# Performance work log

Hardware: AMD Instinct MI355X
Metric: run time of the kernel (lower is better)

The kernel has to match this reference:

```python
import jax, jax.numpy as jnp
import numpy as np

B, S, D, H, E = 4, 2048, 512, 8, 4  # batch, seq, embed, heads, expand
HD = D // H


def setup_inputs() -> dict:
    key = jax.random.key(0)
    ks = jax.random.split(key, 9)
    s = lambda k, shape, fan: jax.random.normal(k, shape, jnp.float32) * (fan ** -0.5)
    return {
        "x": jax.random.normal(ks[0], (B, S, D), jnp.float32),
        "Wq": s(ks[1], (D, D), D),
        "Wk": s(ks[2], (D, D), D),
        "Wv": s(ks[3], (D, D), D),
        "Wo": s(ks[4], (D, D), D),
        "W1": s(ks[5], (D, D * E), D),
        "b1": jnp.zeros((D * E,), jnp.float32),
        "W2": s(ks[6], (D * E, D), D * E),
        "b2": jnp.zeros((D,), jnp.float32),
    }


def _encoder_layer(x, Wq, Wk, Wv, Wo, W1, b1, W2, b2):
    # NOTE: source computes InstanceNorm1d twice but discards both results -> no-ops.
    scale = D ** -0.25  # applied to BOTH q and k (net 1/sqrt(embed_dim))
    q = (x @ Wq).reshape(B, S, H, HD).transpose(0, 2, 1, 3) * scale  # [B,H,S,hd]
    k = (x @ Wk).reshape(B, S, H, HD).transpose(0, 2, 1, 3) * scale
    v = (x @ Wv).reshape(B, S, H, HD).transpose(0, 2, 1, 3)
    scores = jnp.einsum('bhqd,bhkd->bhqk', q, k)  # [B,H,S,S]
    attn = jax.nn.softmax(scores, axis=-1)
    o = jnp.einsum('bhqk,bhkd->bhqd', attn, v)  # [B,H,S,hd]
    o = o.transpose(0, 2, 1, 3).reshape(B, S, D)
    x = o @ Wo + x  # residual 1
    h = jax.nn.gelu(x @ W1 + b1, approximate=True)  # torch GELU(approximate='tanh')
    return h @ W2 + b2 + x  # residual 2 (dropout=0, eval)


def reference(x, Wq, Wk, Wv, Wo, W1, b1, W2, b2):
    return _encoder_layer(x, Wq, Wk, Wv, Wo, W1, b1, W2, b2)
```

## Files before the change

kernel.cpp:

```cpp
#include <hip/hip_runtime.h>
#include <hip/hip_bf16.h>


typedef __bf16 bf16;
typedef __attribute__((ext_vector_type(8))) __bf16 bf16x8;
typedef __attribute__((ext_vector_type(4))) __bf16 bf16x4;
typedef __attribute__((ext_vector_type(4))) float f32x4;
typedef __attribute__((ext_vector_type(16))) float f32x16;
typedef __attribute__((ext_vector_type(4))) short s16x4;
typedef __attribute__((ext_vector_type(2))) unsigned int u32x2;
typedef __attribute__((ext_vector_type(4))) unsigned int u32x4;

#define LOG2E 1.4426950408889634f
#define SCORE_SCALE 0.044194173824159216f
#define SCALE_L2E (SCORE_SCALE * LOG2E)
#define FIXED_M 12.0f

#if __has_builtin(__builtin_amdgcn_exp2f)
#define EXP2(x) __builtin_amdgcn_exp2f(x)
#else
#define EXP2(x) exp2f(x)
#endif

__device__ __forceinline__ void gl_lds16(const bf16* g, bf16* l) {
  __builtin_amdgcn_global_load_lds(
      (const __attribute__((address_space(1))) unsigned int*)g,
      (__attribute__((address_space(3))) unsigned int*)l, 16, 0, 0);
}

__device__ __forceinline__ float gelu_tanh(float x) {
  float u = 0.7978845608028654f * (x + 0.044715f * x * x * x);
  float e = EXP2(u * (2.0f * LOG2E));
  float th = 1.0f - 2.0f / (e + 1.0f);
  return 0.5f * x * (1.0f + th);
}

__device__ __forceinline__ f32x4 mfma_bf16(bf16x8 a, bf16x8 b, f32x4 c) {
  return __builtin_amdgcn_mfma_f32_16x16x32_bf16(a, b, c, 0, 0, 0);
}
__device__ __forceinline__ f32x16 mfma32x16(bf16x8 a, bf16x8 b, f32x16 c) {
  return __builtin_amdgcn_mfma_f32_32x32x16_bf16(a, b, c, 0, 0, 0);
}

__device__ __forceinline__ void plswap(unsigned int& a, unsigned int& b) {
  asm volatile("v_permlane32_swap_b32 %0, %1" : "+v"(a), "+v"(b));
}

template <int MODE, typename OutT, int TN>
__global__ __launch_bounds__(256, 2) void gemm_bt(
    const bf16* __restrict__ A, const bf16* __restrict__ Bt,
    OutT* __restrict__ C, const float* __restrict__ bias,
    const float* __restrict__ resf, const bf16* __restrict__ resb,
    int M, int N, int K) {
  constexpr int MI = (TN == 128) ? 4 : 2;
  __shared__ __align__(16) bf16 sA[2][128 * 32];
  __shared__ __align__(16) bf16 sB[2][TN * 32];
  const int tid = threadIdx.x;
  const int lane = tid & 63;
  const int quad = lane >> 4, lc = lane & 15;
  const int wave = tid >> 6;
  const int wr = (TN == 128) ? (wave >> 1) : wave;
  const int wc = (TN == 128) ? (wave & 1) : 0;
  const int m0 = blockIdx.y * 128, n0 = blockIdx.x * TN;

  const int srow = tid >> 2;
  const int kc = (tid & 3) * 8;
  const bf16* Ag1 = A + (size_t)(m0 + srow) * K + kc;
  const bf16* Ag2 = A + (size_t)(m0 + 64 + srow) * K + kc;
  const bf16* Bg1 = Bt + (size_t)(n0 + srow) * K + kc;
  const bf16* Bg2 = Bt + (size_t)(n0 + 64 + srow) * K + kc;
  const int o1 = tid * 8, o2 = (tid + 256) * 8;

  f32x4 acc[MI][4];
#pragma unroll
  for (int mi = 0; mi < MI; ++mi)
#pragma unroll
    for (int ni = 0; ni < 4; ++ni) acc[mi][ni] = (f32x4){0.f, 0.f, 0.f, 0.f};

  gl_lds16(Ag1, sA[0] + o1);
  gl_lds16(Ag2, sA[0] + o2);
  gl_lds16(Bg1, sB[0] + o1);
  if (TN == 128) gl_lds16(Bg2, sB[0] + o2);
  Ag1 += 32; Ag2 += 32; Bg1 += 32; Bg2 += 32;

  const int kIters = K >> 5;
  for (int kt = 0; kt < kIters; ++kt) {
    __syncthreads();
    const bf16* cA = sA[kt & 1];
    const bf16* cB = sB[kt & 1];
    if (kt + 1 < kIters) {
      bf16* nA = sA[(kt + 1) & 1];
      bf16* nB = sB[(kt + 1) & 1];
      gl_lds16(Ag1, nA + o1);
      gl_lds16(Ag2, nA + o2);
      gl_lds16(Bg1, nB + o1);
      if (TN == 128) gl_lds16(Bg2, nB + o2);
      Ag1 += 32; Ag2 += 32; Bg1 += 32; Bg2 += 32;
    }

    bf16x8 af[MI], bfm[4];
#pragma unroll
    for (int i = 0; i < MI; ++i)
      af[i] =
          *(const bf16x8*)(cA + ((wr * (16 * MI) + i * 16 + lc) * 32 + quad * 8));
#pragma unroll
    for (int i = 0; i < 4; ++i)
      bfm[i] = *(const bf16x8*)(cB + ((wc * 64 + i * 16 + lc) * 32 + quad * 8));
#pragma unroll
    for (int mi = 0; mi < MI; ++mi)
#pragma unroll
      for (int ni = 0; ni < 4; ++ni)
        acc[mi][ni] = mfma_bf16(af[mi], bfm[ni], acc[mi][ni]);
  }

#pragma unroll
  for (int mi = 0; mi < MI; ++mi) {
#pragma unroll
    for (int r = 0; r < 4; ++r) {
      const int row = m0 + wr * (16 * MI) + mi * 16 + quad * 4 + r;
#pragma unroll
      for (int ni = 0; ni < 4; ++ni) {
        const int col = n0 + wc * 64 + ni * 16 + lc;
        const size_t idx = (size_t)row * N + col;
        float v = acc[mi][ni][r];
        if (MODE == 1) v += resf[idx];
        if (MODE == 2) v = gelu_tanh(v + bias[col]);
        if (MODE == 3) v += bias[col] + (float)resb[idx];
        C[idx] = (OutT)v;
      }
    }
  }
}

__global__ __launch_bounds__(256, 2) void flash_attn(
    const bf16* __restrict__ QKV, const bf16* __restrict__ Vt,
    bf16* __restrict__ O) {
  const int tid = threadIdx.x;
  const int lane = tid & 63, wave = tid >> 6;
  const int lo5 = lane & 31, hi = lane >> 5;
  const int lin = blockIdx.y * 16 + blockIdx.x;
  const int xcd = lin & 7, slot = lin >> 3;
  const int bh = xcd * 4 + (slot >> 4);
  const int qt = slot & 15;
  const int b = bh >> 3, h = bh & 7;
  const int q0 = qt * 128 + wave * 32;

  __shared__ __align__(16) bf16 sK[3][4096];
  __shared__ __align__(16) bf16 sV[4][4096];

  const bf16* Qrow = QKV + (size_t)(b * 2048 + q0 + lo5) * 1536 + h * 64;
  bf16x8 qf[4];
#pragma unroll
  for (int i = 0; i < 4; ++i) qf[i] = *(const bf16x8*)(Qrow + i * 16 + hi * 8);

  const int colsw = (((lane & 7) ^ (lane >> 3)) << 3);
  const bf16* Kg0 = QKV + (size_t)b * 2048 * 1536 + 512 + (size_t)h * 64 +
                    (size_t)(wave * 16 + (lane >> 3)) * 1536 + colsw;
  const bf16* Vg0 = Vt + (size_t)bh * 64 * 2048 +
                    (size_t)(wave * 16 + (lane >> 3)) * 2048 + colsw;
  const int stag = wave * 1024;
  const int m7 = lo5 & 7;

  f32x16 oacc[2];
  oacc[0] = (f32x16)(0.f);
  oacc[1] = (f32x16)(0.f);
  float rsum = 0.f;

  auto stage = [&](int t) {
    bf16* dk = sK[t % 3] + stag;
    bf16* dv = sV[t & 3] + stag;
    gl_lds16(Kg0 + (size_t)t * 64 * 1536, dk);
    gl_lds16(Kg0 + (size_t)(t * 64 + 8) * 1536, dk + 512);
    gl_lds16(Vg0 + t * 64, dv);
    gl_lds16(Vg0 + t * 64 + 8 * 2048, dv + 512);
  };

  bf16x8 paw[4];

  auto qk_softmax = [&](const bf16* cK) {
#pragma unroll
    for (int hl = 0; hl < 2; ++hl) {
      const int R = hl * 32 + lo5;
      bf16x8 kf0 = *(const bf16x8*)(cK + R * 64 + (((0 + hi) ^ m7) << 3));
      bf16x8 kf1 = *(const bf16x8*)(cK + R * 64 + (((2 + hi) ^ m7) << 3));
      bf16x8 kf2 = *(const bf16x8*)(cK + R * 64 + (((4 + hi) ^ m7) << 3));
      bf16x8 kf3 = *(const bf16x8*)(cK + R * 64 + (((6 + hi) ^ m7) << 3));
      f32x16 st0 = (f32x16)(0.f), st1 = (f32x16)(0.f);
      __builtin_amdgcn_s_setprio(1);
      st0 = mfma32x16(kf0, qf[0], st0);
      st1 = mfma32x16(kf1, qf[1], st1);
      st0 = mfma32x16(kf2, qf[2], st0);
      st1 = mfma32x16(kf3, qf[3], st1);
      __builtin_amdgcn_s_setprio(0);
      f32x16 st = st0 + st1;
      unsigned int q32[4][2];
#pragma unroll
      for (int g = 0; g < 4; ++g) {
        bf16x4 pb;
#pragma unroll
        for (int j = 0; j < 4; ++j) {
          float p = EXP2(st[4 * g + j] * SCALE_L2E - FIXED_M);
          rsum += p;
          pb[j] = (bf16)p;
        }
        u32x2 w2 = __builtin_bit_cast(u32x2, pb);
        q32[g][0] = w2[0];
        q32[g][1] = w2[1];
      }
#pragma unroll
      for (int t = 0; t < 2; ++t) {
        unsigned int a0 = q32[2 * t][0], a1 = q32[2 * t][1];
        unsigned int b0 = q32[2 * t + 1][0], b1 = q32[2 * t + 1][1];
        plswap(a0, b0);
        plswap(a1, b1);
        u32x4 f = {a0, a1, b0, b1};
        paw[hl * 2 + t] = __builtin_bit_cast(bf16x8, f);
      }
    }
  };

  auto pv = [&](const bf16* cV) {
    __builtin_amdgcn_s_setprio(1);
#pragma unroll
    for (int dh = 0; dh < 2; ++dh) {
      const int Rd = dh * 32 + lo5;
#pragma unroll
      for (int w = 0; w < 4; ++w) {
        bf16x8 vf =
            *(const bf16x8*)(cV + Rd * 64 + (((2 * w + hi) ^ m7) << 3));
        oacc[dh] = mfma32x16(paw[w], vf, oacc[dh]);
      }
    }
    __builtin_amdgcn_s_setprio(0);
  };

  stage(0);
  stage(1);
  asm volatile("s_waitcnt vmcnt(4)\ns_barrier" ::: "memory");
  stage(2);
  qk_softmax(sK[0]);

  for (int kt = 1; kt < 32; ++kt) {
    if (kt == 31)
      asm volatile("s_waitcnt vmcnt(0)\ns_barrier" ::: "memory");
    else
      asm volatile("s_waitcnt vmcnt(4)\ns_barrier" ::: "memory");
    if (kt + 2 < 32) stage(kt + 2);
    const bf16* cK = sK[kt % 3];
    const bf16* cVp = sV[(kt + 3) & 3];
    pv(cVp);
    qk_softmax(cK);
  }
  pv(sV[31 & 3]);

  rsum += __shfl_xor(rsum, 32, 64);
  const size_t obase = (size_t)(b * 2048 + q0) * 512 + h * 64;
#pragma unroll
  for (int r = 0; r < 16; ++r) {
    const int qloc = (r & 3) + 8 * (r >> 2) + 4 * hi;
    const float inv = 1.0f / __shfl(rsum, qloc, 64);
#pragma unroll
    for (int dh = 0; dh < 2; ++dh)
      O[obase + (size_t)qloc * 512 + dh * 32 + lo5] =
          (bf16)(oacc[dh][r] * inv);
  }
}

__global__ __launch_bounds__(256) void prep(
    const float* __restrict__ x, const float* __restrict__ Wq,
    const float* __restrict__ Wk, const float* __restrict__ Wv,
    const float* __restrict__ Wo, const float* __restrict__ W1,
    const float* __restrict__ W2, bf16* __restrict__ xb,
    bf16* __restrict__ WqkvT, bf16* __restrict__ WoT, bf16* __restrict__ W1T,
    bf16* __restrict__ W2T) {
  const int bid = blockIdx.x;
  if (bid < 4096) {
    const size_t i = ((size_t)bid * 256 + threadIdx.x) * 4;
    const float4 v = *(const float4*)(x + i);
    bf16x4 o;
    o[0] = (bf16)v.x; o[1] = (bf16)v.y; o[2] = (bf16)v.z; o[3] = (bf16)v.w;
    *(bf16x4*)(xb + i) = o;
    return;
  }
  const int t = bid - 4096;
  const float* in;
  bf16* out;
  int in_ld, out_ld, bx, by;
  if (t < 1024) {
    const int q = t >> 8, r = t & 255;
    bx = r & 15; by = r >> 4; in_ld = 512; out_ld = 512;
    in = (q == 0) ? Wq : (q == 1) ? Wk : (q == 2) ? Wv : Wo;
    out = (q == 0) ? WqkvT
          : (q == 1) ? WqkvT + 512 * 512
          : (q == 2) ? WqkvT + 2 * 512 * 512
                     : WoT;
  } else if (t < 2048) {
    const int r = t - 1024;
    bx = r & 63; by = r >> 6; in_ld = 2048; out_ld = 512;
    in = W1; out = W1T;
  } else {
    const int r = t - 2048;
    bx = r & 15; by = r >> 4; in_ld = 512; out_ld = 2048;
    in = W2; out = W2T;
  }
  __shared__ __align__(16) bf16 tl[32][33];
  const int tx = threadIdx.x & 31, ty = threadIdx.x >> 5;
  const int n0 = bx * 32, k0 = by * 32;
#pragma unroll
  for (int i = 0; i < 4; ++i)
    tl[ty + 8 * i][tx] = (bf16)in[(size_t)(k0 + ty + 8 * i) * in_ld + n0 + tx];
  __syncthreads();
#pragma unroll
  for (int i = 0; i < 4; ++i)
    out[(size_t)(n0 + ty + 8 * i) * out_ld + k0 + tx] = tl[tx][ty + 8 * i];
}

__global__ __launch_bounds__(256) void transpose_v(
    const bf16* __restrict__ QKV, bf16* __restrict__ Vt) {
  __shared__ __align__(16) bf16 t[32][33];
  const int tx = threadIdx.x & 31, ty = threadIdx.x >> 5;
  const int bh = blockIdx.z, b = bh >> 3, h = bh & 7;
  const bf16* ip = QKV + (size_t)b * 2048 * 1536 + 1024 + h * 64;
  bf16* op = Vt + (size_t)bh * 64 * 2048;
  const int d0 = blockIdx.x * 32, s0 = blockIdx.y * 32;
#pragma unroll
  for (int i = 0; i < 4; ++i)
    t[ty + 8 * i][tx] = ip[(size_t)(s0 + ty + 8 * i) * 1536 + d0 + tx];
  __syncthreads();
#pragma unroll
  for (int i = 0; i < 4; ++i)
    op[(size_t)(d0 + ty + 8 * i) * 2048 + s0 + tx] = t[tx][ty + 8 * i];
}

extern "C" void kernel_launch(void* const* d_in, const int* in_sizes, int n_in,
                              void* d_out, int out_size, void* d_ws,
                              size_t ws_size, hipStream_t stream) {
  const float* x = (const float*)d_in[0];
  const float* Wq = (const float*)d_in[1];
  const float* Wk = (const float*)d_in[2];
  const float* Wv = (const float*)d_in[3];
  const float* Wo = (const float*)d_in[4];
  const float* W1 = (const float*)d_in[5];
  const float* b1 = (const float*)d_in[6];
  const float* W2 = (const float*)d_in[7];
  const float* b2 = (const float*)d_in[8];
  float* out = (float*)d_out;

  char* ws = (char*)d_ws;
  size_t off = 0;
  auto alloc = [&](size_t bytes) {
    char* p = ws + off;
    off += (bytes + 255) & ~(size_t)255;
    return p;
  };
  bf16* WqkvT = (bf16*)alloc(1536ULL * 512 * 2);
  bf16* WoT = (bf16*)alloc(512ULL * 512 * 2);
  bf16* W1T = (bf16*)alloc(2048ULL * 512 * 2);
  bf16* W2T = (bf16*)alloc(512ULL * 2048 * 2);
  bf16* xb = (bf16*)alloc(8192ULL * 512 * 2);
  bf16* QKV = (bf16*)alloc(8192ULL * 1536 * 2);
  bf16* Vt = (bf16*)alloc(32ULL * 64 * 2048 * 2);
  bf16* attn = (bf16*)alloc(8192ULL * 512 * 2);
  bf16* x2 = xb;
  bf16* hbuf = QKV;

  const dim3 tb(256);
  prep<<<dim3(7168), tb, 0, stream>>>(x, Wq, Wk, Wv, Wo, W1, W2, xb, WqkvT,
                                      WoT, W1T, W2T);
  gemm_bt<0, bf16, 128><<<dim3(12, 64), tb, 0, stream>>>(
      xb, WqkvT, QKV, nullptr, nullptr, nullptr, 8192, 1536, 512);
  transpose_v<<<dim3(2, 64, 32), tb, 0, stream>>>(QKV, Vt);
  flash_attn<<<dim3(16, 32), tb, 0, stream>>>(QKV, Vt, attn);
  gemm_bt<1, bf16, 64><<<dim3(8, 64), tb, 0, stream>>>(
      attn, WoT, x2, nullptr, x, nullptr, 8192, 512, 512);
  gemm_bt<2, bf16, 128><<<dim3(16, 64), tb, 0, stream>>>(
      x2, W1T, hbuf, b1, nullptr, nullptr, 8192, 2048, 512);
  gemm_bt<3, float, 64><<<dim3(8, 64), tb, 0, stream>>>(
      hbuf, W2T, out, b2, nullptr, x2, 8192, 512, 2048);
}
```

Before: 257.5 us.

## Triple-buffer GEMM loads and restructure flash attention loop without software pipelining

The GEMM moves from a double-buffered LDS pipeline with __syncthreads to a three-stage ring with a two-tiles-ahead prefetch and explicit vmcnt waits plus barrier, aiming to hide global load latency. Flash attention drops the skewed schedule, where PV of the previous tile overlapped QK/softmax of the current one, in favour of a plain per-tile loop. That loop preloads V fragments, chains the QK MFMAs into a single accumulator and splits the row-sum into four partial accumulators. V LDS buffers shrink from four to three. The trade-off is more LDS per GEMM block and a flash loop that loses the overlap between PV and softmax.

```diff
diff --git a/kernel.cpp b/kernel.cpp
--- a/kernel.cpp
+++ b/kernel.cpp
@@ -7,7 +7,6 @@
 typedef __attribute__((ext_vector_type(4))) __bf16 bf16x4;
 typedef __attribute__((ext_vector_type(4))) float f32x4;
 typedef __attribute__((ext_vector_type(16))) float f32x16;
-typedef __attribute__((ext_vector_type(4))) short s16x4;
 typedef __attribute__((ext_vector_type(2))) unsigned int u32x2;
 typedef __attribute__((ext_vector_type(4))) unsigned int u32x4;
 
@@ -26,6 +25,16 @@
   __builtin_amdgcn_global_load_lds(
       (const __attribute__((address_space(1))) unsigned int*)g,
       (__attribute__((address_space(3))) unsigned int*)l, 16, 0, 0);
+}
+
+template <int N>
+__device__ __forceinline__ void wait_vm_barrier() {
+  if constexpr (N == 0)
+    asm volatile("s_waitcnt vmcnt(0)\ns_barrier" ::: "memory");
+  else if constexpr (N == 3)
+    asm volatile("s_waitcnt vmcnt(3)\ns_barrier" ::: "memory");
+  else if constexpr (N == 4)
+    asm volatile("s_waitcnt vmcnt(4)\ns_barrier" ::: "memory");
 }
 
 __device__ __forceinline__ float gelu_tanh(float x) {
@@ -53,8 +62,9 @@
     const float* __restrict__ resf, const bf16* __restrict__ resb,
     int M, int N, int K) {
   constexpr int MI = (TN == 128) ? 4 : 2;
-  __shared__ __align__(16) bf16 sA[2][128 * 32];
-  __shared__ __align__(16) bf16 sB[2][TN * 32];
+  constexpr int L = (TN == 128) ? 4 : 3;
+  __shared__ __align__(16) bf16 sA[3][128 * 32];
+  __shared__ __align__(16) bf16 sB[3][TN * 32];
   const int tid = threadIdx.x;
   const int lane = tid & 63;
   const int quad = lane >> 4, lc = lane & 15;
@@ -77,26 +87,27 @@
 #pragma unroll
     for (int ni = 0; ni < 4; ++ni) acc[mi][ni] = (f32x4){0.f, 0.f, 0.f, 0.f};
 
-  gl_lds16(Ag1, sA[0] + o1);
-  gl_lds16(Ag2, sA[0] + o2);
-  gl_lds16(Bg1, sB[0] + o1);
-  if (TN == 128) gl_lds16(Bg2, sB[0] + o2);
-  Ag1 += 32; Ag2 += 32; Bg1 += 32; Bg2 += 32;
+  auto stage = [&](int t) {
+    bf16* a = sA[t % 3];
+    bf16* bb = sB[t % 3];
+    gl_lds16(Ag1 + t * 32, a + o1);
+    gl_lds16(Ag2 + t * 32, a + o2);
+    gl_lds16(Bg1 + t * 32, bb + o1);
+    if (TN == 128) gl_lds16(Bg2 + t * 32, bb + o2);
+  };
 
   const int kIters = K >> 5;
+  stage(0);
+  stage(1);
+
   for (int kt = 0; kt < kIters; ++kt) {
-    __syncthreads();
-    const bf16* cA = sA[kt & 1];
-    const bf16* cB = sB[kt & 1];
-    if (kt + 1 < kIters) {
-      bf16* nA = sA[(kt + 1) & 1];
-      bf16* nB = sB[(kt + 1) & 1];
-      gl_lds16(Ag1, nA + o1);
-      gl_lds16(Ag2, nA + o2);
-      gl_lds16(Bg1, nB + o1);
-      if (TN == 128) gl_lds16(Bg2, nB + o2);
-      Ag1 += 32; Ag2 += 32; Bg1 += 32; Bg2 += 32;
-    }
+    if (kt + 1 < kIters)
+      wait_vm_barrier<L>();
+    else
+      wait_vm_barrier<0>();
+    if (kt + 2 < kIters) stage(kt + 2);
+    const bf16* cA = sA[kt % 3];
+    const bf16* cB = sB[kt % 3];
 
     bf16x8 af[MI], bfm[4];
 #pragma unroll
@@ -146,7 +157,7 @@
   const int q0 = qt * 128 + wave * 32;
 
   __shared__ __align__(16) bf16 sK[3][4096];
-  __shared__ __align__(16) bf16 sV[4][4096];
+  __shared__ __align__(16) bf16 sV[3][4096];
 
   const bf16* Qrow = QKV + (size_t)(b * 2048 + q0 + lo5) * 1536 + h * 64;
   bf16x8 qf[4];
@@ -164,45 +175,61 @@
   f32x16 oacc[2];
   oacc[0] = (f32x16)(0.f);
   oacc[1] = (f32x16)(0.f);
-  float rsum = 0.f;
+  float rs0 = 0.f, rs1 = 0.f, rs2 = 0.f, rs3 = 0.f;
 
   auto stage = [&](int t) {
     bf16* dk = sK[t % 3] + stag;
-    bf16* dv = sV[t & 3] + stag;
+    bf16* dv = sV[t % 3] + stag;
     gl_lds16(Kg0 + (size_t)t * 64 * 1536, dk);
     gl_lds16(Kg0 + (size_t)(t * 64 + 8) * 1536, dk + 512);
     gl_lds16(Vg0 + t * 64, dv);
     gl_lds16(Vg0 + t * 64 + 8 * 2048, dv + 512);
   };
-
-  bf16x8 paw[4];
-
-  auto qk_softmax = [&](const bf16* cK) {
+  stage(0);
+  stage(1);
+
+  for (int kt = 0; kt < 32; ++kt) {
+    if (kt == 31)
+      wait_vm_barrier<0>();
+    else
+      wait_vm_barrier<4>();
+    if (kt + 2 < 32) stage(kt + 2);
+    const bf16* cK = sK[kt % 3];
+    const bf16* cV = sV[kt % 3];
+
+    bf16x8 vf[2][4];
+#pragma unroll
+    for (int dh = 0; dh < 2; ++dh) {
+      const int Rd = dh * 32 + lo5;
+#pragma unroll
+      for (int w = 0; w < 4; ++w)
+        vf[dh][w] =
+            *(const bf16x8*)(cV + Rd * 64 + (((2 * w + hi) ^ m7) << 3));
+    }
+
+    bf16x8 paw[4];
 #pragma unroll
     for (int hl = 0; hl < 2; ++hl) {
+      f32x16 st = (f32x16)(0.f);
       const int R = hl * 32 + lo5;
-      bf16x8 kf0 = *(const bf16x8*)(cK + R * 64 + (((0 + hi) ^ m7) << 3));
-      bf16x8 kf1 = *(const bf16x8*)(cK + R * 64 + (((2 + hi) ^ m7) << 3));
-      bf16x8 kf2 = *(const bf16x8*)(cK + R * 64 + (((4 + hi) ^ m7) << 3));
-      bf16x8 kf3 = *(const bf16x8*)(cK + R * 64 + (((6 + hi) ^ m7) << 3));
-      f32x16 st0 = (f32x16)(0.f), st1 = (f32x16)(0.f);
       __builtin_amdgcn_s_setprio(1);
-      st0 = mfma32x16(kf0, qf[0], st0);
-      st1 = mfma32x16(kf1, qf[1], st1);
-      st0 = mfma32x16(kf2, qf[2], st0);
-      st1 = mfma32x16(kf3, qf[3], st1);
+#pragma unroll
+      for (int i = 0; i < 4; ++i) {
+        bf16x8 kf =
+            *(const bf16x8*)(cK + R * 64 + (((2 * i + hi) ^ m7) << 3));
+        st = mfma32x16(kf, qf[i], st);
+      }
       __builtin_amdgcn_s_setprio(0);
-      f32x16 st = st0 + st1;
       unsigned int q32[4][2];
 #pragma unroll
       for (int g = 0; g < 4; ++g) {
         bf16x4 pb;
-#pragma unroll
-        for (int j = 0; j < 4; ++j) {
-          float p = EXP2(st[4 * g + j] * SCALE_L2E - FIXED_M);
-          rsum += p;
-          pb[j] = (bf16)p;
-        }
+        float p0 = EXP2(st[4 * g + 0] * SCALE_L2E - FIXED_M);
+        float p1 = EXP2(st[4 * g + 1] * SCALE_L2E - FIXED_M);
+        float p2 = EXP2(st[4 * g + 2] * SCALE_L2E - FIXED_M);
+        float p3 = EXP2(st[4 * g + 3] * SCALE_L2E - FIXED_M);
+        rs0 += p0; rs1 += p1; rs2 += p2; rs3 += p3;
+        pb[0] = (bf16)p0; pb[1] = (bf16)p1; pb[2] = (bf16)p2; pb[3] = (bf16)p3;
         u32x2 w2 = __builtin_bit_cast(u32x2, pb);
         q32[g][0] = w2[0];
         q32[g][1] = w2[1];
@@ -217,42 +244,17 @@
         paw[hl * 2 + t] = __builtin_bit_cast(bf16x8, f);
       }
     }
-  };
-
-  auto pv = [&](const bf16* cV) {
+
     __builtin_amdgcn_s_setprio(1);
 #pragma unroll
-    for (int dh = 0; dh < 2; ++dh) {
-      const int Rd = dh * 32 + lo5;
-#pragma unroll
-      for (int w = 0; w < 4; ++w) {
-        bf16x8 vf =
-            *(const bf16x8*)(cV + Rd * 64 + (((2 * w + hi) ^ m7) << 3));
-        oacc[dh] = mfma32x16(paw[w], vf, oacc[dh]);
-      }
-    }
+    for (int dh = 0; dh < 2; ++dh)
+#pragma unroll
+      for (int w = 0; w < 4; ++w)
+        oacc[dh] = mfma32x16(paw[w], vf[dh][w], oacc[dh]);
     __builtin_amdgcn_s_setprio(0);
-  };
-
-  stage(0);
-  stage(1);
-  asm volatile("s_waitcnt vmcnt(4)\ns_barrier" ::: "memory");
-  stage(2);
-  qk_softmax(sK[0]);
-
-  for (int kt = 1; kt < 32; ++kt) {
-    if (kt == 31)
-      asm volatile("s_waitcnt vmcnt(0)\ns_barrier" ::: "memory");
-    else
-      asm volatile("s_waitcnt vmcnt(4)\ns_barrier" ::: "memory");
-    if (kt + 2 < 32) stage(kt + 2);
-    const bf16* cK = sK[kt % 3];
-    const bf16* cVp = sV[(kt + 3) & 3];
-    pv(cVp);
-    qk_softmax(cK);
-  }
-  pv(sV[31 & 3]);
-
+  }
+
+  float rsum = (rs0 + rs1) + (rs2 + rs3);
   rsum += __shfl_xor(rsum, 32, 64);
   const size_t obase = (size_t)(b * 2048 + q0) * 512 + h * 64;
 #pragma unroll
```

Measured after the change: 257.5 us. No clear change (-0.0%).
